# Kernel optimization log

Measured on AMD Instinct MI355X. Metric: run time of the kernel, lower is better.

Reference implementation:

```python
import jax, jax.numpy as jnp
import numpy as np

DIM, NH, WS, SS, MLP_RATIO = 192, 6, 8, 4, 4
EPS = 1e-5


def _rel_pos_index(ws):
    coords = np.stack(np.meshgrid(np.arange(ws), np.arange(ws), indexing='ij')).reshape(2, -1)
    rel = (coords[:, :, None] - coords[:, None, :]).transpose(1, 2, 0)
    rel[:, :, 0] += ws - 1
    rel[:, :, 1] += ws - 1
    rel[:, :, 0] *= 2 * ws - 1
    return rel.sum(-1)  # (ws*ws, ws*ws) int


def _attn_mask(hp, wp, ws, ss):
    img = np.zeros((hp, wp))
    slices = (slice(0, -ws), slice(-ws, -ss), slice(-ss, None))
    cnt = 0
    for hs in slices:
        for vs in slices:
            img[hs, vs] = cnt
            cnt += 1
    mw = img.reshape(hp // ws, ws, wp // ws, ws).transpose(0, 2, 1, 3).reshape(-1, ws * ws)
    am = mw[:, None, :] - mw[:, :, None]  # (nW, N, N)
    return jnp.asarray(np.where(am != 0, -100.0, 0.0).astype(np.float32))


def _ln(x, g, b):
    mu = jnp.mean(x, axis=-1, keepdims=True)
    var = jnp.mean(jnp.square(x - mu), axis=-1, keepdims=True)
    return (x - mu) * jax.lax.rsqrt(var + EPS) * g + b


def setup_inputs():
    key = jax.random.key(0)
    ks = jax.random.split(key, 8)
    B, H, W, C = 8, 128, 128, DIM
    hid = C * MLP_RATIO
    n = lambda k, s: jax.random.normal(k, s, dtype=jnp.float32) * 0.02
    return {
        'x': jax.random.normal(ks[0], (B, H * W, C), dtype=jnp.float32),
        'h': H, 'w': W,
        'norm1_g': jnp.ones((C,), jnp.float32), 'norm1_b': jnp.zeros((C,), jnp.float32),
        'qkv_w': n(ks[1], (C, 3 * C)), 'qkv_b': jnp.zeros((3 * C,), jnp.float32),
        'proj_w': n(ks[2], (C, C)), 'proj_b': jnp.zeros((C,), jnp.float32),
        'rel_bias_table': n(ks[3], ((2 * WS - 1) ** 2, NH)),
        'norm2_g': jnp.ones((C,), jnp.float32), 'norm2_b': jnp.zeros((C,), jnp.float32),
        'fc1_w': n(ks[4], (C, hid)), 'fc1_b': jnp.zeros((hid,), jnp.float32),
        'fc2_w': n(ks[5], (hid, C)), 'fc2_b': jnp.zeros((C,), jnp.float32),
    }


def reference(x, h, w, norm1_g, norm1_b, qkv_w, qkv_b, proj_w, proj_b,
              rel_bias_table, norm2_g, norm2_b, fc1_w, fc1_b, fc2_w, fc2_b):
    B, L, C = x.shape
    ws, ss, nh = WS, SS, NH
    hd = C // nh
    scale = hd ** (-0.5)

    shortcut = x
    xg = _ln(x, norm1_g, norm1_b).reshape(B, h, w, C)

    pad_h = (-h) % ws
    pad_w = (-w) % ws
    if pad_h or pad_w:
        xg = jnp.pad(xg, ((0, 0), (0, pad_h), (0, pad_w), (0, 0)))
    hp, wp = h + pad_h, w + pad_w
    if ss > 0:
        xg = jnp.roll(xg, (-ss, -ss), axis=(1, 2))

    # window partition -> (nB, N, C)
    win = xg.reshape(B, hp // ws, ws, wp // ws, ws, C).transpose(0, 1, 3, 2, 4, 5).reshape(-1, ws * ws, C)
    nB, N, _ = win.shape

    qkv = (win @ qkv_w + qkv_b).reshape(nB, N, 3, nh, hd).transpose(2, 0, 3, 1, 4)
    q, k, v = qkv[0] * scale, qkv[1], qkv[2]  # (nB, nh, N, hd)

    attn = jnp.einsum('bhnd,bhmd->bhnm', q, k)  # (nB, nh, N, N)
    rpi = _rel_pos_index(ws)
    bias = rel_bias_table[rpi.reshape(-1)].reshape(N, N, nh).transpose(2, 0, 1)
    attn = attn + bias[None]
    if ss > 0:
        mask = _attn_mask(hp, wp, ws, ss)  # (nW, N, N)
        nW = mask.shape[0]
        attn = (attn.reshape(nB // nW, nW, nh, N, N) + mask[None, :, None]).reshape(nB, nh, N, N)
    attn = jax.nn.softmax(attn, axis=-1)

    out = jnp.einsum('bhnm,bhmd->bnhd', attn, v).reshape(nB, N, C)
    out = out @ proj_w + proj_b

    # window reverse
    out = out.reshape(B, hp // ws, wp // ws, ws, ws, C).transpose(0, 1, 3, 2, 4, 5).reshape(B, hp, wp, C)
    if ss > 0:
        out = jnp.roll(out, (ss, ss), axis=(1, 2))
    out = out[:, :h, :w].reshape(B, h * w, C)

    x = shortcut + out
    xn2 = _ln(x, norm2_g, norm2_b)
    mlp = jax.nn.gelu(xn2 @ fc1_w + fc1_b, approximate=False) @ fc2_w + fc2_b
    return x + mlp
```

## Files before the change

kernel.cpp:

```cpp
#include <hip/hip_runtime.h>

typedef unsigned short u16;
typedef unsigned int   u32;
typedef __attribute__((ext_vector_type(8))) short bf16x8;
typedef __attribute__((ext_vector_type(4))) float f32x4;

#define L_TOK   16384
#define C_DIM   192
#define HID_DIM 768

#define OFF_QKV  0
#define OFF_PROJ 110592
#define OFF_FC1  147456
#define OFF_FC2  294912
#define CVT_TOT  442368

union FragU { int4 i4; bf16x8 h8; };

#define MFMA_B16(a,b,c) __builtin_amdgcn_mfma_f32_16x16x32_bf16(a,b,c,0,0,0)

__device__ __forceinline__ u16 f2bf(float f) {
    u32 t; __builtin_memcpy(&t, &f, 4);
    t += 0x7FFFu + ((t >> 16) & 1u);
    return (u16)(t >> 16);
}

__global__ __launch_bounds__(256) void k_cvt(
    const float* __restrict__ qkvw, const float* __restrict__ projw,
    const float* __restrict__ fc1w, const float* __restrict__ fc2w,
    u16* __restrict__ ws)
{
    const int i = blockIdx.x * 256 + threadIdx.x;
    if (i >= CVT_TOT) return;
    float v; int dst;
    if (i < OFF_PROJ) {
        const int k = i / 576, col = i % 576;
        const int grp = col / 192, rem = col % 192;
        const int head = rem >> 5, dim = rem & 31;
        v = qkvw[i];
        dst = OFF_QKV + head * (96 * 192) + (grp * 32 + dim) * 192 + k;
    } else if (i < OFF_FC1) {
        const int s = i - OFF_PROJ;
        const int cin = s / 192, cout = s % 192;
        const int head = cin >> 5, j = cin & 31;
        v = projw[s];
        dst = OFF_PROJ + head * (192 * 32) + cout * 32 + j;
    } else if (i < OFF_FC2) {
        const int s = i - OFF_FC1;
        const int k = s / 768, h = s % 768;
        v = fc1w[s];
        const int hc = h / 96, cc = h % 96;
        const int kc = k >> 6, ko = k & 63;
        const int q = cc * 64 + (ko ^ ((cc & 7) << 3));
        dst = OFF_FC1 + (hc * 3 + kc) * 6144 + q;
    } else {
        const int s = i - OFF_FC2;
        const int h = s / 192, c = s % 192;
        v = fc2w[s];
        const int hc = h / 96, rem = h % 96;
        const int sc = rem >> 5, ho = rem & 31;
        const int q = c * 32 + (ho ^ ((c & 3) << 3));
        dst = OFF_FC2 + (hc * 3 + sc) * 6144 + q;
    }
    ws[dst] = f2bf(v);
}

__global__ __launch_bounds__(256, 2) void k_attnproj(
    const float* __restrict__ x, const float* __restrict__ g1v, const float* __restrict__ b1v,
    const u16* __restrict__ qkvwT, const float* __restrict__ qkvb,
    const float* __restrict__ relb, const u16* __restrict__ projT, const float* __restrict__ projb,
    float* __restrict__ x1)
{
    struct PW {
        u16 qsb[64 * 40];
        u16 ksb[64 * 40];
        u16 vsbT[32 * 72];
        u16 psb[64 * 72];
        u16 oh [64 * 40];
    };
    union SmemU {
        u16 xw[128 * 200];
        PW pw[2];
    };
    __shared__ __align__(16) SmemU u;
    __shared__ __align__(16) u16 wbuf[192 * 40];
    __shared__ float relbs[225 * 6];

    const int t  = threadIdx.x;
    const int lane = t & 63, w = t >> 6;
    const int win = w >> 1, half = w & 1;
    const int l15 = lane & 15, quad = lane >> 4;
    const int wi2 = blockIdx.x * 2 + win;
    const int b  = wi2 >> 8;
    const int hb = (wi2 >> 4) & 15;
    const int wb = wi2 & 15;
    const bool maskon = (hb == 15) || (wb == 15);
    const f32x4 zf = {0.f, 0.f, 0.f, 0.f};

    for (int i = t; i < 225 * 6; i += 256) relbs[i] = relb[i];

    #pragma unroll
    for (int tk = 0; tk < 2; ++tk) {
        const int nn = t >> 2, q4 = t & 3;
        const int tok = tk * 64 + nn;
        const int tw = tok >> 6, n = tok & 63;
        const int wiA = blockIdx.x * 2 + tw;
        const int bA  = wiA >> 8;
        const int hbA = (wiA >> 4) & 15, wbA = wiA & 15;
        const int r = n >> 3, c = n & 7;
        const int ho = (hbA * 8 + r + 4) & 127;
        const int wo = (wbA * 8 + c + 4) & 127;
        const size_t xoff = ((size_t)bA * L_TOK + ho * 128 + wo) * C_DIM;
        const float* xp = x + xoff + q4 * 48;
        float f[48];
        float sum = 0.f, sq = 0.f;
        #pragma unroll
        for (int i = 0; i < 12; ++i) {
            float4 v = *(const float4*)(xp + i * 4);
            f[i*4+0]=v.x; f[i*4+1]=v.y; f[i*4+2]=v.z; f[i*4+3]=v.w;
            sum += v.x+v.y+v.z+v.w;
            sq  += v.x*v.x + v.y*v.y + v.z*v.z + v.w*v.w;
        }
        sum += __shfl_xor(sum, 1); sum += __shfl_xor(sum, 2);
        sq  += __shfl_xor(sq, 1);  sq  += __shfl_xor(sq, 2);
        const float mu = sum * (1.f / 192.f);
        const float rstd = rsqrtf(sq * (1.f / 192.f) - mu * mu + 1e-5f);
        u16* xrow = u.xw + tok * 200 + q4 * 48;
        #pragma unroll
        for (int i = 0; i < 6; ++i) {
            u32 pk[4];
            #pragma unroll
            for (int j = 0; j < 4; ++j) {
                float g0 = g1v[q4*48 + i*8 + j*2],     b0 = b1v[q4*48 + i*8 + j*2];
                float g1 = g1v[q4*48 + i*8 + j*2 + 1], b1 = b1v[q4*48 + i*8 + j*2 + 1];
                float y0 = (f[i*8+j*2]   - mu) * rstd * g0 + b0;
                float y1 = (f[i*8+j*2+1] - mu) * rstd * g1 + b1;
                pk[j] = (u32)f2bf(y0) | (((u32)f2bf(y1)) << 16);
            }
            *(int4*)(xrow + i * 8) = make_int4((int)pk[0], (int)pk[1], (int)pk[2], (int)pk[3]);
        }
    }
    __syncthreads();

    FragU afrag[2][6];
    #pragma unroll
    for (int mt = 0; mt < 2; ++mt)
        #pragma unroll
        for (int kk = 0; kk < 6; ++kk)
            afrag[mt][kk].i4 = *(const int4*)(u.xw +
                (win*64 + half*32 + mt*16 + l15) * 200 + kk*32 + quad*8);

    PW* P = &u.pw[win];
    const int rb = half*32 + quad*4;

    int4 wr0, wr1, wr2;
    auto LOADW = [&](int hh, int sub) {
        if (sub < 3) {
            const u16* src = qkvwT + (size_t)hh * (96 * 192) + sub * 64;
            wr0 = *(const int4*)(src + ((t      ) >> 3) * 192 + ((t      ) & 7) * 8);
            wr1 = *(const int4*)(src + ((t + 256) >> 3) * 192 + ((t + 256) & 7) * 8);
            wr2 = *(const int4*)(src + ((t + 512) >> 3) * 192 + ((t + 512) & 7) * 8);
        } else {
            const u16* src = projT + (size_t)hh * (192 * 32);
            wr0 = *(const int4*)(src + ((t      ) >> 2) * 32 + ((t      ) & 3) * 8);
            wr1 = *(const int4*)(src + ((t + 256) >> 2) * 32 + ((t + 256) & 3) * 8);
            wr2 = *(const int4*)(src + ((t + 512) >> 2) * 32 + ((t + 512) & 3) * 8);
        }
    };
    auto STOREW = [&](int sub) {
        if (sub < 3) {
            *(int4*)(wbuf + ((t      ) >> 3) * 72 + ((t      ) & 7) * 8) = wr0;
            *(int4*)(wbuf + ((t + 256) >> 3) * 72 + ((t + 256) & 7) * 8) = wr1;
            *(int4*)(wbuf + ((t + 512) >> 3) * 72 + ((t + 512) & 7) * 8) = wr2;
        } else {
            *(int4*)(wbuf + ((t      ) >> 2) * 40 + ((t      ) & 3) * 8) = wr0;
            *(int4*)(wbuf + ((t + 256) >> 2) * 40 + ((t + 256) & 3) * 8) = wr1;
            *(int4*)(wbuf + ((t + 512) >> 2) * 40 + ((t + 512) & 3) * 8) = wr2;
        }
    };
    LOADW(0, 0);

    f32x4 acc2[2][12];
    #pragma unroll
    for (int mt = 0; mt < 2; ++mt)
        #pragma unroll
        for (int nt = 0; nt < 12; ++nt) acc2[mt][nt] = zf;

    for (int head = 0; head < 6; ++head) {
        f32x4 accq[2][6];
        #pragma unroll
        for (int mt = 0; mt < 2; ++mt)
            #pragma unroll
            for (int nt = 0; nt < 6; ++nt) accq[mt][nt] = zf;

        for (int kc = 0; kc < 3; ++kc) {
            __syncthreads();
            STOREW(kc);
            __syncthreads();
            LOADW(head, kc + 1);
            #pragma unroll
            for (int s = 0; s < 2; ++s) {
                #pragma unroll
                for (int nt = 0; nt < 6; ++nt) {
                    FragU bf_;
                    bf_.i4 = *(const int4*)(wbuf + (nt*16 + l15)*72 + s*32 + quad*8);
                    accq[0][nt] = MFMA_B16(afrag[0][kc*2 + s].h8, bf_.h8, accq[0][nt]);
                    accq[1][nt] = MFMA_B16(afrag[1][kc*2 + s].h8, bf_.h8, accq[1][nt]);
                }
            }
        }
        #pragma unroll
        for (int mt = 0; mt < 2; ++mt) {
            #pragma unroll
            for (int nt = 0; nt < 6; ++nt) {
                const int grp = nt >> 1;
                const int dim = (nt & 1)*16 + l15;
                const float bias = qkvb[grp*192 + head*32 + dim];
                float vv[4];
                #pragma unroll
                for (int rg = 0; rg < 4; ++rg) vv[rg] = accq[mt][nt][rg] + bias;
                const int rowb = rb + mt*16;
                if (grp == 0) {
                    #pragma unroll
                    for (int rg = 0; rg < 4; ++rg)
                        P->qsb[(rowb + rg)*40 + dim] = f2bf(vv[rg] * 0.17677669529663687f);
                } else if (grp == 1) {
                    #pragma unroll
                    for (int rg = 0; rg < 4; ++rg)
                        P->ksb[(rowb + rg)*40 + dim] = f2bf(vv[rg]);
                } else {
                    u32 lo = (u32)f2bf(vv[0]) | (((u32)f2bf(vv[1])) << 16);
                    u32 hi = (u32)f2bf(vv[2]) | (((u32)f2bf(vv[3])) << 16);
                    *(uint2*)&P->vsbT[dim*72 + rowb] = make_uint2(lo, hi);
                }
            }
        }
        __syncthreads();

        FragU qf0, qf1;
        qf0.i4 = *(const int4*)(P->qsb + (half*32 + l15)*40 + quad*8);
        qf1.i4 = *(const int4*)(P->qsb + (half*32 + 16 + l15)*40 + quad*8);
        f32x4 sv[2][4];
        #pragma unroll
        for (int nt = 0; nt < 4; ++nt) {
            FragU kf; kf.i4 = *(const int4*)(P->ksb + (nt*16 + l15)*40 + quad*8);
            sv[0][nt] = MFMA_B16(qf0.h8, kf.h8, zf);
            sv[1][nt] = MFMA_B16(qf1.h8, kf.h8, zf);
        }
        const int kr_ = l15 >> 3, kc2 = l15 & 7;
        #pragma unroll
        for (int mt = 0; mt < 2; ++mt) {
            #pragma unroll
            for (int rg = 0; rg < 4; ++rg) {
                const int qm = rb + mt*16 + rg;
                const int qr = qm >> 3, qc = qm & 7;
                #pragma unroll
                for (int nt = 0; nt < 4; ++nt) {
                    const int kr = nt*2 + kr_;
                    sv[mt][nt][rg] += relbs[((qr - kr + 7)*15 + (qc - kc2 + 7))*6 + head];
                }
            }
        }
        if (maskon) {
            #pragma unroll
            for (int mt = 0; mt < 2; ++mt) {
                #pragma unroll
                for (int rg = 0; rg < 4; ++rg) {
                    const int qm = rb + mt*16 + rg;
                    const int qr = qm >> 3, qc = qm & 7;
                    const int regq = ((hb == 15) ? (qr < 4 ? 1 : 2) : 0) * 3
                                   + ((wb == 15) ? (qc < 4 ? 1 : 2) : 0);
                    #pragma unroll
                    for (int nt = 0; nt < 4; ++nt) {
                        const int kr = nt*2 + kr_;
                        const int regk = ((hb == 15) ? (kr < 4 ? 1 : 2) : 0) * 3
                                       + ((wb == 15) ? (kc2 < 4 ? 1 : 2) : 0);
                        if (regq != regk) sv[mt][nt][rg] -= 100.f;
                    }
                }
            }
        }
        #pragma unroll
        for (int mt = 0; mt < 2; ++mt) {
            #pragma unroll
            for (int rg = 0; rg < 4; ++rg) {
                float mx = fmaxf(fmaxf(sv[mt][0][rg], sv[mt][1][rg]),
                                 fmaxf(sv[mt][2][rg], sv[mt][3][rg]));
                mx = fmaxf(mx, __shfl_xor(mx, 1));
                mx = fmaxf(mx, __shfl_xor(mx, 2));
                mx = fmaxf(mx, __shfl_xor(mx, 4));
                mx = fmaxf(mx, __shfl_xor(mx, 8));
                float s0 = 0.f;
                #pragma unroll
                for (int nt = 0; nt < 4; ++nt) {
                    sv[mt][nt][rg] = __expf(sv[mt][nt][rg] - mx); s0 += sv[mt][nt][rg];
                }
                s0 += __shfl_xor(s0, 1); s0 += __shfl_xor(s0, 2);
                s0 += __shfl_xor(s0, 4); s0 += __shfl_xor(s0, 8);
                const float inv = 1.f / s0;
                #pragma unroll
                for (int nt = 0; nt < 4; ++nt)
                    P->psb[(rb + mt*16 + rg)*72 + nt*16 + l15] = f2bf(sv[mt][nt][rg] * inv);
            }
        }

        FragU vb[2][2];
        #pragma unroll
        for (int ntv = 0; ntv < 2; ++ntv) {
            vb[ntv][0].i4 = *(const int4*)(P->vsbT + (ntv*16 + l15)*72 + quad*8);
            vb[ntv][1].i4 = *(const int4*)(P->vsbT + (ntv*16 + l15)*72 + 32 + quad*8);
        }
        #pragma unroll
        for (int mt = 0; mt < 2; ++mt) {
            FragU pa0, pa1;
            pa0.i4 = *(const int4*)(P->psb + (half*32 + mt*16 + l15)*72 + quad*8);
            pa1.i4 = *(const int4*)(P->psb + (half*32 + mt*16 + l15)*72 + 32 + quad*8);
            f32x4 ov0 = zf, ov1 = zf;
            ov0 = MFMA_B16(pa0.h8, vb[0][0].h8, ov0);
            ov0 = MFMA_B16(pa1.h8, vb[0][1].h8, ov0);
            ov1 = MFMA_B16(pa0.h8, vb[1][0].h8, ov1);
            ov1 = MFMA_B16(pa1.h8, vb[1][1].h8, ov1);
            #pragma unroll
            for (int rg = 0; rg < 4; ++rg) {
                P->oh[(rb + mt*16 + rg)*40 + l15]      = f2bf(ov0[rg]);
                P->oh[(rb + mt*16 + rg)*40 + 16 + l15] = f2bf(ov1[rg]);
            }
        }

        STOREW(3);
        __syncthreads();
        if (head < 5) LOADW(head + 1, 0);
        FragU ao0, ao1;
        ao0.i4 = *(const int4*)(P->oh + (half*32 + l15)*40 + quad*8);
        ao1.i4 = *(const int4*)(P->oh + (half*32 + 16 + l15)*40 + quad*8);
        #pragma unroll
        for (int nt = 0; nt < 12; ++nt) {
            FragU bp; bp.i4 = *(const int4*)(wbuf + (nt*16 + l15)*40 + quad*8);
            acc2[0][nt] = MFMA_B16(ao0.h8, bp.h8, acc2[0][nt]);
            acc2[1][nt] = MFMA_B16(ao1.h8, bp.h8, acc2[1][nt]);
        }
    }

    {
        float pb[12];
        #pragma unroll
        for (int nt = 0; nt < 12; ++nt) pb[nt] = projb[nt*16 + l15];
        #pragma unroll
        for (int mt = 0; mt < 2; ++mt) {
            #pragma unroll
            for (int rg = 0; rg < 4; ++rg) {
                const int tok = rb + mt*16 + rg;
                const int tr = tok >> 3, tc = tok & 7;
                const int ho2 = (hb * 8 + tr + 4) & 127;
                const int wo2 = (wb * 8 + tc + 4) & 127;
                const size_t base = ((size_t)b * L_TOK + ho2 * 128 + wo2) * C_DIM;
                #pragma unroll
                for (int nt = 0; nt < 12; ++nt) {
                    const int col = nt*16 + l15;
                    x1[base + col] = acc2[mt][nt][rg] + pb[nt] + x[base + col];
                }
            }
        }
    }
}

__global__ __launch_bounds__(256, 2) void k_mlp(
    const float* x1, const float* __restrict__ g2v, const float* __restrict__ b2v,
    const u16* __restrict__ fc1wT, const float* __restrict__ fc1b,
    const u16* __restrict__ fc2wT, const float* __restrict__ fc2b,
    float* out)
{
    union SmemU {
        u16 xnA[64 * 200];
        u16 hbuf[128 * 104];
    };
    __shared__ __align__(16) SmemU u;
    __shared__ __align__(16) u16 wbig[2][6144];

    const int blk = blockIdx.x;
    const int t = threadIdx.x;
    const size_t row0 = (size_t)blk * 128;
    const int lane = t & 63, w = t >> 6;
    const int l15 = lane & 15, quad = lane >> 4;
    const f32x4 zf = {0.f, 0.f, 0.f, 0.f};

    auto issue_stage = [&](int st) {
        const int hcs = st / 6, sub = st % 6;
        const u16* src = (sub < 3) ? fc1wT + (hcs * 3 + sub) * 6144
                                   : fc2wT + (hcs * 3 + (sub - 3)) * 6144;
        u16* dstb = &wbig[st & 1][0];
        #pragma unroll
        for (int c = 0; c < 3; ++c) {
            const int cid = c * 4 + w;
            __builtin_amdgcn_global_load_lds(
                (const __attribute__((address_space(1))) void*)(src + cid * 512 + lane * 8),
                (__attribute__((address_space(3))) void*)(dstb + cid * 512),
                16, 0, 0);
        }
    };
    issue_stage(0);

    FragU afrag[2][6];
    for (int hf = 0; hf < 2; ++hf) {
        const int nn = t >> 2, q4 = t & 3;
        const int tok = hf * 64 + nn;
        const float* xp = x1 + (row0 + tok) * C_DIM + q4 * 48;
        float f[48];
        float sum = 0.f, sq = 0.f;
        #pragma unroll
        for (int i = 0; i < 12; ++i) {
            float4 v = *(const float4*)(xp + i * 4);
            f[i*4+0]=v.x; f[i*4+1]=v.y; f[i*4+2]=v.z; f[i*4+3]=v.w;
            sum += v.x+v.y+v.z+v.w;
            sq  += v.x*v.x + v.y*v.y + v.z*v.z + v.w*v.w;
        }
        sum += __shfl_xor(sum,1); sum += __shfl_xor(sum,2);
        sq  += __shfl_xor(sq,1);  sq  += __shfl_xor(sq,2);
        const float mu = sum * (1.f/192.f);
        const float rstd = rsqrtf(sq * (1.f/192.f) - mu*mu + 1e-5f);
        u16* xrow = u.xnA + nn * 200 + q4 * 48;
        #pragma unroll
        for (int i = 0; i < 6; ++i) {
            u32 pk[4];
            #pragma unroll
            for (int j = 0; j < 4; ++j) {
                float g0 = g2v[q4*48 + i*8 + j*2],     b0 = b2v[q4*48 + i*8 + j*2];
                float g1 = g2v[q4*48 + i*8 + j*2 + 1], b1 = b2v[q4*48 + i*8 + j*2 + 1];
                float y0 = (f[i*8+j*2]   - mu) * rstd * g0 + b0;
                float y1 = (f[i*8+j*2+1] - mu) * rstd * g1 + b1;
                pk[j] = (u32)f2bf(y0) | (((u32)f2bf(y1)) << 16);
            }
            *(int4*)(xrow + i*8) = make_int4((int)pk[0], (int)pk[1], (int)pk[2], (int)pk[3]);
        }
        __syncthreads();
        #pragma unroll
        for (int kk = 0; kk < 6; ++kk)
            afrag[hf][kk].i4 = *(const int4*)(u.xnA + (w*16 + l15) * 200 + kk*32 + quad*8);
        __syncthreads();
    }

    f32x4 acc2[2][12];
    #pragma unroll
    for (int mt = 0; mt < 2; ++mt)
        #pragma unroll
        for (int nt = 0; nt < 12; ++nt) acc2[mt][nt] = zf;

    int g = 0;
    for (int hc = 0; hc < 8; ++hc) {
        f32x4 acc1[2][6];
        #pragma unroll
        for (int mt = 0; mt < 2; ++mt)
            #pragma unroll
            for (int nt = 0; nt < 6; ++nt) acc1[mt][nt] = zf;

        for (int kc = 0; kc < 3; ++kc) {
            __syncthreads();
            if (g < 47) issue_stage(g + 1);
            const u16* buf = &wbig[g & 1][0];
            #pragma unroll
            for (int s = 0; s < 2; ++s) {
                #pragma unroll
                for (int nt = 0; nt < 6; ++nt) {
                    const int row = nt*16 + l15;
                    FragU bf_;
                    bf_.i4 = *(const int4*)(buf + row*64 +
                                            ((s*32 + quad*8) ^ ((row & 7) << 3)));
                    acc1[0][nt] = MFMA_B16(afrag[0][kc*2 + s].h8, bf_.h8, acc1[0][nt]);
                    acc1[1][nt] = MFMA_B16(afrag[1][kc*2 + s].h8, bf_.h8, acc1[1][nt]);
                }
            }
            ++g;
        }
        #pragma unroll
        for (int nt = 0; nt < 6; ++nt) {
            const float bb = fc1b[hc*96 + nt*16 + l15];
            #pragma unroll
            for (int mt = 0; mt < 2; ++mt) {
                #pragma unroll
                for (int rg = 0; rg < 4; ++rg) {
                    float h = acc1[mt][nt][rg] + bb;
                    float e = __expf(h * (-1.5957691216057308f
                                          - 0.0713548162726302f * h * h));
                    float gl = h / (1.f + e);
                    u.hbuf[(mt*64 + w*16 + quad*4 + rg) * 104 + nt*16 + l15] = f2bf(gl);
                }
            }
        }
        for (int sc = 0; sc < 3; ++sc) {
            __syncthreads();
            if (g < 47) issue_stage(g + 1);
            const u16* buf = &wbig[g & 1][0];
            FragU ha0, ha1;
            ha0.i4 = *(const int4*)(u.hbuf + (w*16 + l15) * 104 + sc*32 + quad*8);
            ha1.i4 = *(const int4*)(u.hbuf + (64 + w*16 + l15) * 104 + sc*32 + quad*8);
            #pragma unroll
            for (int nt = 0; nt < 12; ++nt) {
                const int row = nt*16 + l15;
                FragU bf_;
                bf_.i4 = *(const int4*)(buf + row*32 +
                                        ((quad*8) ^ ((row & 3) << 3)));
                acc2[0][nt] = MFMA_B16(ha0.h8, bf_.h8, acc2[0][nt]);
                acc2[1][nt] = MFMA_B16(ha1.h8, bf_.h8, acc2[1][nt]);
            }
            ++g;
        }
    }

    #pragma unroll
    for (int nt = 0; nt < 12; ++nt) {
        const int col = nt*16 + l15;
        const float bb = fc2b[col];
        #pragma unroll
        for (int mt = 0; mt < 2; ++mt) {
            #pragma unroll
            for (int rg = 0; rg < 4; ++rg) {
                const size_t idx = (row0 + mt*64 + w*16 + quad*4 + rg) * C_DIM + col;
                out[idx] = acc2[mt][nt][rg] + bb + x1[idx];
            }
        }
    }
}

extern "C" void kernel_launch(void* const* d_in, const int* in_sizes, int n_in,
                              void* d_out, int out_size, void* d_ws, size_t ws_size,
                              hipStream_t stream) {
    const float* x     = (const float*)d_in[0];
    const float* g1v   = (const float*)d_in[3];
    const float* b1v   = (const float*)d_in[4];
    const float* qkvw  = (const float*)d_in[5];
    const float* qkvb  = (const float*)d_in[6];
    const float* projw = (const float*)d_in[7];
    const float* projb = (const float*)d_in[8];
    const float* relb  = (const float*)d_in[9];
    const float* g2v   = (const float*)d_in[10];
    const float* b2v   = (const float*)d_in[11];
    const float* fc1w  = (const float*)d_in[12];
    const float* fc1b  = (const float*)d_in[13];
    const float* fc2w  = (const float*)d_in[14];
    const float* fc2b  = (const float*)d_in[15];

    float* x1 = (float*)d_out;
    u16* wsb  = (u16*)d_ws;

    hipLaunchKernelGGL(k_cvt, dim3((CVT_TOT + 255) / 256), dim3(256), 0, stream,
                       qkvw, projw, fc1w, fc2w, wsb);
    hipLaunchKernelGGL(k_attnproj, dim3(1024), dim3(256), 0, stream,
                       x, g1v, b1v, wsb + OFF_QKV, qkvb, relb, wsb + OFF_PROJ, projb, x1);
    hipLaunchKernelGGL(k_mlp, dim3(1024), dim3(256), 0, stream,
                       x1, g2v, b2v, wsb + OFF_FC1, fc1b, wsb + OFF_FC2, fc2b, x1);
}
```

Before: 513.6 us.

## Stream attention weights into double-buffered swizzled LDS via direct global-to-LDS loads

Replaces the register-staged weight loads (global load to registers, then a store to padded LDS) in the attention/projection kernel with `global_load_lds` into a two-slot LDS buffer. The next QKV or projection weight stage is issued while the current one is consumed, which removes one barrier per stage. The conversion kernel now writes the QKV and proj weights in an XOR-swizzled tile layout so fragment reads from the unpadded LDS tiles avoid bank conflicts. The Q and per-head output scratch buffers are merged to save LDS. This raises the weight-buffer LDS footprint and relies on the asynchronous LDS writes being complete by the barrier.

```diff
diff --git a/kernel.cpp b/kernel.cpp
--- a/kernel.cpp
+++ b/kernel.cpp
@@ -38,29 +38,29 @@
         const int grp = col / 192, rem = col % 192;
         const int head = rem >> 5, dim = rem & 31;
         v = qkvw[i];
-        dst = OFF_QKV + head * (96 * 192) + (grp * 32 + dim) * 192 + k;
+        const int cc = grp * 32 + dim;
+        const int kc = k >> 6, ko = k & 63;
+        dst = OFF_QKV + (head * 3 + kc) * 6144 + cc * 64 + (ko ^ ((cc & 7) << 3));
     } else if (i < OFF_FC1) {
         const int s = i - OFF_PROJ;
         const int cin = s / 192, cout = s % 192;
         const int head = cin >> 5, j = cin & 31;
         v = projw[s];
-        dst = OFF_PROJ + head * (192 * 32) + cout * 32 + j;
+        dst = OFF_PROJ + head * 6144 + cout * 32 + (j ^ ((cout & 3) << 3));
     } else if (i < OFF_FC2) {
         const int s = i - OFF_FC1;
         const int k = s / 768, h = s % 768;
         v = fc1w[s];
         const int hc = h / 96, cc = h % 96;
         const int kc = k >> 6, ko = k & 63;
-        const int q = cc * 64 + (ko ^ ((cc & 7) << 3));
-        dst = OFF_FC1 + (hc * 3 + kc) * 6144 + q;
+        dst = OFF_FC1 + (hc * 3 + kc) * 6144 + cc * 64 + (ko ^ ((cc & 7) << 3));
     } else {
         const int s = i - OFF_FC2;
         const int h = s / 192, c = s % 192;
         v = fc2w[s];
         const int hc = h / 96, rem = h % 96;
         const int sc = rem >> 5, ho = rem & 31;
-        const int q = c * 32 + (ho ^ ((c & 3) << 3));
-        dst = OFF_FC2 + (hc * 3 + sc) * 6144 + q;
+        dst = OFF_FC2 + (hc * 3 + sc) * 6144 + c * 32 + (ho ^ ((c & 3) << 3));
     }
     ws[dst] = f2bf(v);
 }
@@ -72,18 +72,17 @@
     float* __restrict__ x1)
 {
     struct PW {
-        u16 qsb[64 * 40];
+        u16 qoh[64 * 40];
         u16 ksb[64 * 40];
         u16 vsbT[32 * 72];
         u16 psb[64 * 72];
-        u16 oh [64 * 40];
     };
     union SmemU {
         u16 xw[128 * 200];
         PW pw[2];
     };
     __shared__ __align__(16) SmemU u;
-    __shared__ __align__(16) u16 wbuf[192 * 40];
+    __shared__ __align__(16) u16 wdb[2][6144];
     __shared__ float relbs[225 * 6];
 
     const int t  = threadIdx.x;
@@ -96,6 +95,22 @@
     const int wb = wi2 & 15;
     const bool maskon = (hb == 15) || (wb == 15);
     const f32x4 zf = {0.f, 0.f, 0.f, 0.f};
+
+    auto issue_stage = [&](int st) {
+        const int hs = st >> 2, sub = st & 3;
+        const u16* src = (sub < 3) ? qkvwT + (hs * 3 + sub) * 6144
+                                   : projT + hs * 6144;
+        u16* dstb = &wdb[st & 1][0];
+        #pragma unroll
+        for (int c = 0; c < 3; ++c) {
+            const int cid = c * 4 + w;
+            __builtin_amdgcn_global_load_lds(
+                (const __attribute__((address_space(1))) void*)(src + cid * 512 + lane * 8),
+                (__attribute__((address_space(3))) void*)(dstb + cid * 512),
+                16, 0, 0);
+        }
+    };
+    issue_stage(0);
 
     for (int i = t; i < 225 * 6; i += 256) relbs[i] = relb[i];
 
@@ -153,39 +168,13 @@
     PW* P = &u.pw[win];
     const int rb = half*32 + quad*4;
 
-    int4 wr0, wr1, wr2;
-    auto LOADW = [&](int hh, int sub) {
-        if (sub < 3) {
-            const u16* src = qkvwT + (size_t)hh * (96 * 192) + sub * 64;
-            wr0 = *(const int4*)(src + ((t      ) >> 3) * 192 + ((t      ) & 7) * 8);
-            wr1 = *(const int4*)(src + ((t + 256) >> 3) * 192 + ((t + 256) & 7) * 8);
-            wr2 = *(const int4*)(src + ((t + 512) >> 3) * 192 + ((t + 512) & 7) * 8);
-        } else {
-            const u16* src = projT + (size_t)hh * (192 * 32);
-            wr0 = *(const int4*)(src + ((t      ) >> 2) * 32 + ((t      ) & 3) * 8);
-            wr1 = *(const int4*)(src + ((t + 256) >> 2) * 32 + ((t + 256) & 3) * 8);
-            wr2 = *(const int4*)(src + ((t + 512) >> 2) * 32 + ((t + 512) & 3) * 8);
-        }
-    };
-    auto STOREW = [&](int sub) {
-        if (sub < 3) {
-            *(int4*)(wbuf + ((t      ) >> 3) * 72 + ((t      ) & 7) * 8) = wr0;
-            *(int4*)(wbuf + ((t + 256) >> 3) * 72 + ((t + 256) & 7) * 8) = wr1;
-            *(int4*)(wbuf + ((t + 512) >> 3) * 72 + ((t + 512) & 7) * 8) = wr2;
-        } else {
-            *(int4*)(wbuf + ((t      ) >> 2) * 40 + ((t      ) & 3) * 8) = wr0;
-            *(int4*)(wbuf + ((t + 256) >> 2) * 40 + ((t + 256) & 3) * 8) = wr1;
-            *(int4*)(wbuf + ((t + 512) >> 2) * 40 + ((t + 512) & 3) * 8) = wr2;
-        }
-    };
-    LOADW(0, 0);
-
     f32x4 acc2[2][12];
     #pragma unroll
     for (int mt = 0; mt < 2; ++mt)
         #pragma unroll
         for (int nt = 0; nt < 12; ++nt) acc2[mt][nt] = zf;
 
+    int g = 0;
     for (int head = 0; head < 6; ++head) {
         f32x4 accq[2][6];
         #pragma unroll
@@ -195,19 +184,21 @@
 
         for (int kc = 0; kc < 3; ++kc) {
             __syncthreads();
-            STOREW(kc);
-            __syncthreads();
-            LOADW(head, kc + 1);
+            issue_stage(g + 1);
+            const u16* buf = &wdb[g & 1][0];
             #pragma unroll
             for (int s = 0; s < 2; ++s) {
                 #pragma unroll
                 for (int nt = 0; nt < 6; ++nt) {
+                    const int row = nt*16 + l15;
                     FragU bf_;
-                    bf_.i4 = *(const int4*)(wbuf + (nt*16 + l15)*72 + s*32 + quad*8);
+                    bf_.i4 = *(const int4*)(buf + row*64 +
+                                            ((s*32 + quad*8) ^ ((row & 7) << 3)));
                     accq[0][nt] = MFMA_B16(afrag[0][kc*2 + s].h8, bf_.h8, accq[0][nt]);
                     accq[1][nt] = MFMA_B16(afrag[1][kc*2 + s].h8, bf_.h8, accq[1][nt]);
                 }
             }
+            ++g;
         }
         #pragma unroll
         for (int mt = 0; mt < 2; ++mt) {
@@ -223,7 +214,7 @@
                 if (grp == 0) {
                     #pragma unroll
                     for (int rg = 0; rg < 4; ++rg)
-                        P->qsb[(rowb + rg)*40 + dim] = f2bf(vv[rg] * 0.17677669529663687f);
+                        P->qoh[(rowb + rg)*40 + dim] = f2bf(vv[rg] * 0.17677669529663687f);
                 } else if (grp == 1) {
                     #pragma unroll
                     for (int rg = 0; rg < 4; ++rg)
@@ -236,10 +227,11 @@
             }
         }
         __syncthreads();
+        if (head < 5) issue_stage(g + 1);
 
         FragU qf0, qf1;
-        qf0.i4 = *(const int4*)(P->qsb + (half*32 + l15)*40 + quad*8);
-        qf1.i4 = *(const int4*)(P->qsb + (half*32 + 16 + l15)*40 + quad*8);
+        qf0.i4 = *(const int4*)(P->qoh + (half*32 + l15)*40 + quad*8);
+        qf1.i4 = *(const int4*)(P->qoh + (half*32 + 16 + l15)*40 + quad*8);
         f32x4 sv[2][4];
         #pragma unroll
         for (int nt = 0; nt < 4; ++nt) {
@@ -322,23 +314,24 @@
             ov1 = MFMA_B16(pa1.h8, vb[1][1].h8, ov1);
             #pragma unroll
             for (int rg = 0; rg < 4; ++rg) {
-                P->oh[(rb + mt*16 + rg)*40 + l15]      = f2bf(ov0[rg]);
-                P->oh[(rb + mt*16 + rg)*40 + 16 + l15] = f2bf(ov1[rg]);
-            }
-        }
-
-        STOREW(3);
-        __syncthreads();
-        if (head < 5) LOADW(head + 1, 0);
+                P->qoh[(rb + mt*16 + rg)*40 + l15]      = f2bf(ov0[rg]);
+                P->qoh[(rb + mt*16 + rg)*40 + 16 + l15] = f2bf(ov1[rg]);
+            }
+        }
+
+        const u16* pbuf = &wdb[g & 1][0];
         FragU ao0, ao1;
-        ao0.i4 = *(const int4*)(P->oh + (half*32 + l15)*40 + quad*8);
-        ao1.i4 = *(const int4*)(P->oh + (half*32 + 16 + l15)*40 + quad*8);
+        ao0.i4 = *(const int4*)(P->qoh + (half*32 + l15)*40 + quad*8);
+        ao1.i4 = *(const int4*)(P->qoh + (half*32 + 16 + l15)*40 + quad*8);
         #pragma unroll
         for (int nt = 0; nt < 12; ++nt) {
-            FragU bp; bp.i4 = *(const int4*)(wbuf + (nt*16 + l15)*40 + quad*8);
+            const int row = nt*16 + l15;
+            FragU bp;
+            bp.i4 = *(const int4*)(pbuf + row*32 + ((quad*8) ^ ((row & 3) << 3)));
             acc2[0][nt] = MFMA_B16(ao0.h8, bp.h8, acc2[0][nt]);
             acc2[1][nt] = MFMA_B16(ao1.h8, bp.h8, acc2[1][nt]);
         }
+        ++g;
     }
 
     {
```

Result: faster. 489.8 us (-4.6%).
